# Kernel tuning notes

Measured on AMD Instinct MI355X. Metric: run time of the kernel, lower is better.

The kernel has to match this reference:

```python
import jax, jax.numpy as jnp
import numpy as np

N_WIRES = 4
N_LAYERS = 2
PATCHES = 196  # 14x14 grid of 2x2 patches


def _bexp(a, nd):
    # broadcast angle to rank nd by appending singleton axes
    a = jnp.asarray(a)
    return a.reshape(a.shape + (1,) * (nd - a.ndim))


def _apply_ry(state, wire, angle):
    # state: [B, P, 2,2,2,2]; angle broadcastable to [B, P] or scalar
    st = jnp.moveaxis(state, 2 + wire, -1)
    c = _bexp(jnp.cos(angle * 0.5), st.ndim - 1)
    s = _bexp(jnp.sin(angle * 0.5), st.ndim - 1)
    s0, s1 = st[..., 0], st[..., 1]
    out = jnp.stack([c * s0 - s * s1, s * s0 + c * s1], axis=-1)
    return jnp.moveaxis(out, -1, 2 + wire)


def _apply_cnot(state, control, target):
    st = jnp.moveaxis(state, (2 + control, 2 + target), (-2, -1))
    st = jnp.stack([st[..., 0, :], st[..., 1, ::-1]], axis=-2)
    return jnp.moveaxis(st, (-2, -1), (2 + control, 2 + target))


def _measure_z(state):
    # PauliZ expectation on each wire: sum probs * (+1/-1)
    p = state * state  # real state => |amp|^2
    outs = []
    for w in range(N_WIRES):
        axes = tuple(a for a in range(2, 2 + N_WIRES) if a != 2 + w)
        m = p.sum(axis=axes)  # [B, P, 2]
        outs.append(m[..., 0] - m[..., 1])
    return jnp.stack(outs, axis=-1)  # [B, P, 4]


def _quanv(x, theta):
    B = x.shape[0]
    # extract 2x2 patches: order (r,c),(r,c+1),(r+1,c),(r+1,c+1)
    img = x.reshape(B, 14, 2, 14, 2).transpose(0, 1, 3, 2, 4).reshape(B, PATCHES, 4)
    state = jnp.zeros((B, PATCHES, 16), x.dtype).at[:, :, 0].set(1.0)
    state = state.reshape(B, PATCHES, 2, 2, 2, 2)
    # encoder: RY(x_i) on wire i
    for w in range(N_WIRES):
        state = _apply_ry(state, w, img[:, :, w])
    # variational layers: trainable RY per wire + CNOT ring
    for l in range(N_LAYERS):
        for w in range(N_WIRES):
            state = _apply_ry(state, w, theta[l, w])
        for w in range(N_WIRES):
            state = _apply_cnot(state, w, (w + 1) % N_WIRES)
    return _measure_z(state).reshape(B, PATCHES * N_WIRES)  # [B, 784]


def setup_inputs() -> dict:
    key = jax.random.key(0)
    k = jax.random.split(key, 6)
    B = 4096
    return {
        "x": jax.random.uniform(k[0], (B, 784), jnp.float32),
        "theta": jax.random.normal(k[1], (N_LAYERS, N_WIRES), jnp.float32),
        "W1": jax.random.normal(k[2], (784, 128), jnp.float32) * 0.05,
        "b1": jnp.zeros((128,), jnp.float32),
        "W2": jax.random.normal(k[3], (128, 10), jnp.float32) * 0.05,
        "b2": jnp.zeros((10,), jnp.float32),
    }


def reference(x, theta, W1, b1, W2, b2):
    feats = _quanv(x, theta)                 # [B, 784]
    h = jax.nn.relu(feats @ W1 + b1)          # [B, 128]
    logits = h @ W2 + b2                      # [B, 10]
    return jax.nn.log_softmax(logits, axis=-1)
```

## Files before the change

kernel.cpp:

```cpp
#include <hip/hip_runtime.h>
#include <math.h>

#define PATCHES 196
#define KPAD 800
#define MROWS 16
#define CIRC (MROWS * PATCHES)
#define FRAG_ELEMS (25 * 64 * 8)

typedef short short8 __attribute__((ext_vector_type(8)));
typedef float f32x4 __attribute__((ext_vector_type(4)));

__device__ __forceinline__ unsigned short f2bf(float f) {
  union { float f; unsigned u; } x; x.f = f;
  unsigned r = x.u + 0x7fff + ((x.u >> 16) & 1);
  return (unsigned short)(r >> 16);
}

__global__ __launch_bounds__(256) void w1t_pack_kernel(
    const float* __restrict__ W1, unsigned short* __restrict__ w1p) {
  int idx = blockIdx.x * 256 + threadIdx.x;
  if (idx >= 128 * KPAD) return;
  int n = idx / KPAD;
  int k = idx - n * KPAD;
  float v = (k < 784) ? W1[k * 128 + n] : 0.f;
  int ki = k >> 5;
  int quad = (k & 31) >> 3;
  int j = k & 7;
  w1p[(n >> 4) * FRAG_ELEMS + (ki * 64 + quad * 16 + (n & 15)) * 8 + j] = f2bf(v);
}

__device__ __forceinline__ void apply_ry(float st[16], int bit, float c, float s) {
#pragma unroll
  for (int i = 0; i < 16; ++i) {
    if (!(i & bit)) {
      int j = i | bit;
      float a0 = st[i], a1 = st[j];
      st[i] = c * a0 - s * a1;
      st[j] = s * a0 + c * a1;
    }
  }
}

__device__ __forceinline__ void apply_cnot(float st[16], int cb, int tb) {
#pragma unroll
  for (int i = 0; i < 16; ++i) {
    if ((i & cb) && !(i & tb)) {
      int j = i | tb;
      float t = st[i]; st[i] = st[j]; st[j] = t;
    }
  }
}

__global__ __launch_bounds__(1024) void fused_kernel(
    const float* __restrict__ x, const float* __restrict__ theta,
    const unsigned short* __restrict__ w1p, const float* __restrict__ b1,
    const float* __restrict__ W2, const float* __restrict__ b2,
    float* __restrict__ out) {
  __shared__ unsigned short afr[FRAG_ELEMS];
  __shared__ float tc[8], ts[8];
  __shared__ float hs[MROWS * 132];
  __shared__ float ls[MROWS * 10];

  const int tid = threadIdx.x;
  const int row0 = blockIdx.x * MROWS;

  if (tid < 8) {
    float a = 0.5f * theta[tid];
    tc[tid] = __cosf(a);
    ts[tid] = __sinf(a);
  }
  if (tid < 64) {
    int m = tid & 15;
    int qs = tid >> 4;
    int quad = 2 + (qs >> 1);
    int j0 = (qs & 1) * 4;
    ushort4 z; z.x = z.y = z.z = z.w = 0;
    *reinterpret_cast<ushort4*>(afr + (24 * 64 + quad * 16 + m) * 8 + j0) = z;
  }
  __syncthreads();

  for (int c = tid; c < CIRC; c += 1024) {
    int bl = c / PATCHES;
    int p = c - bl * PATCHES;
    int pr = p / 14;
    int pc = p - pr * 14;

    const float* xb = x + (size_t)(row0 + bl) * 784 + pr * 56 + pc * 2;
    float v0 = xb[0], v1 = xb[1], v2 = xb[28], v3 = xb[29];

    float st[16];
#pragma unroll
    for (int i = 0; i < 16; ++i) st[i] = 0.f;
    st[0] = 1.f;

    apply_ry(st, 8, __cosf(0.5f * v0), __sinf(0.5f * v0));
    apply_ry(st, 4, __cosf(0.5f * v1), __sinf(0.5f * v1));
    apply_ry(st, 2, __cosf(0.5f * v2), __sinf(0.5f * v2));
    apply_ry(st, 1, __cosf(0.5f * v3), __sinf(0.5f * v3));

#pragma unroll
    for (int l = 0; l < 2; ++l) {
      apply_ry(st, 8, tc[l * 4 + 0], ts[l * 4 + 0]);
      apply_ry(st, 4, tc[l * 4 + 1], ts[l * 4 + 1]);
      apply_ry(st, 2, tc[l * 4 + 2], ts[l * 4 + 2]);
      apply_ry(st, 1, tc[l * 4 + 3], ts[l * 4 + 3]);
      apply_cnot(st, 8, 4);
      apply_cnot(st, 4, 2);
      apply_cnot(st, 2, 1);
      apply_cnot(st, 1, 8);
    }

    float m0 = 0.f, m1 = 0.f, m2 = 0.f, m3 = 0.f;
#pragma unroll
    for (int i = 0; i < 16; ++i) {
      float p2 = st[i] * st[i];
      m0 += (i & 8) ? -p2 : p2;
      m1 += (i & 4) ? -p2 : p2;
      m2 += (i & 2) ? -p2 : p2;
      m3 += (i & 1) ? -p2 : p2;
    }

    int K = p * 4;
    int ki = K >> 5;
    int quad = (K & 31) >> 3;
    int j0 = K & 7;
    ushort4 o;
    o.x = f2bf(m0); o.y = f2bf(m1); o.z = f2bf(m2); o.w = f2bf(m3);
    *reinterpret_cast<ushort4*>(afr + (ki * 64 + quad * 16 + bl) * 8 + j0) = o;
  }
  __syncthreads();

  const int lane = tid & 63;
  const int wave = tid >> 6;
  const int m = lane & 15;
  const int quad = lane >> 4;

  if (wave < 8) {
    const unsigned short* bp = w1p + (size_t)wave * FRAG_ELEMS + lane * 8;
    const unsigned short* apl = afr + lane * 8;

    f32x4 acc = {0.f, 0.f, 0.f, 0.f};

#pragma unroll
    for (int kc = 0; kc < 5; ++kc) {
      short8 a[5], b[5];
#pragma unroll
      for (int u = 0; u < 5; ++u) {
        const int ki = kc * 5 + u;
        a[u] = *reinterpret_cast<const short8*>(apl + ki * 512);
        b[u] = *reinterpret_cast<const short8*>(bp + ki * 512);
      }
#pragma unroll
      for (int u = 0; u < 5; ++u)
        acc = __builtin_amdgcn_mfma_f32_16x16x32_bf16(a[u], b[u], acc, 0, 0, 0);
    }

    const int col = wave * 16 + m;
    const float bc = b1[col];
#pragma unroll
    for (int r = 0; r < 4; ++r)
      hs[(quad * 4 + r) * 132 + col] = fmaxf(acc[r] + bc, 0.f);
  }
  __syncthreads();

  if (tid < MROWS * 10) {
    const int r = tid / 10;
    const int k = tid - r * 10;
    float a = b2[k];
    const float* hr = hs + r * 132;
#pragma unroll 8
    for (int jj = 0; jj < 128; ++jj) a = fmaf(hr[jj], W2[jj * 10 + k], a);
    ls[tid] = a;
  }
  __syncthreads();

  if (tid < MROWS) {
    const int r = tid;
    float mx = ls[r * 10];
#pragma unroll
    for (int k = 1; k < 10; ++k) mx = fmaxf(mx, ls[r * 10 + k]);
    float sum = 0.f;
#pragma unroll
    for (int k = 0; k < 10; ++k) sum += __expf(ls[r * 10 + k] - mx);
    const float lse = mx + __logf(sum);
    float* orow = out + (size_t)(row0 + r) * 10;
#pragma unroll
    for (int k = 0; k < 10; ++k) orow[k] = ls[r * 10 + k] - lse;
  }
}

extern "C" void kernel_launch(void* const* d_in, const int* in_sizes, int n_in,
                              void* d_out, int out_size, void* d_ws, size_t ws_size,
                              hipStream_t stream) {
  const float* x     = (const float*)d_in[0];
  const float* theta = (const float*)d_in[1];
  const float* W1    = (const float*)d_in[2];
  const float* b1    = (const float*)d_in[3];
  const float* W2    = (const float*)d_in[4];
  const float* b2    = (const float*)d_in[5];
  float* out = (float*)d_out;

  const int B = in_sizes[0] / 784;

  unsigned short* w1p = (unsigned short*)d_ws;

  w1t_pack_kernel<<<(128 * KPAD + 255) / 256, 256, 0, stream>>>(W1, w1p);
  fused_kernel<<<B / MROWS, 1024, 0, stream>>>(x, theta, w1p, b1, W2, b2, out);
}
```

Baseline: 89.49 us.

## Halve rows per block, prefetch inputs into registers, stage W2 in LDS

```diff
diff --git a/kernel.cpp b/kernel.cpp
--- a/kernel.cpp
+++ b/kernel.cpp
@@ -3,8 +3,9 @@
 
 #define PATCHES 196
 #define KPAD 800
-#define MROWS 16
+#define MROWS 8
 #define CIRC (MROWS * PATCHES)
+#define THREADS 512
 #define FRAG_ELEMS (25 * 64 * 8)
 
 typedef short short8 __attribute__((ext_vector_type(8)));
@@ -51,46 +52,61 @@
   }
 }
 
-__global__ __launch_bounds__(1024) void fused_kernel(
+__global__ __launch_bounds__(THREADS) void fused_kernel(
     const float* __restrict__ x, const float* __restrict__ theta,
     const unsigned short* __restrict__ w1p, const float* __restrict__ b1,
     const float* __restrict__ W2, const float* __restrict__ b2,
     float* __restrict__ out) {
   __shared__ unsigned short afr[FRAG_ELEMS];
   __shared__ float tc[8], ts[8];
+  __shared__ float ws2[1280];
   __shared__ float hs[MROWS * 132];
   __shared__ float ls[MROWS * 10];
 
   const int tid = threadIdx.x;
   const int row0 = blockIdx.x * MROWS;
 
+  {
+    ushort4 z; z.x = z.y = z.z = z.w = 0;
+    for (int s = tid; s < FRAG_ELEMS / 4; s += THREADS)
+      reinterpret_cast<ushort4*>(afr)[s] = z;
+  }
   if (tid < 8) {
     float a = 0.5f * theta[tid];
     tc[tid] = __cosf(a);
     ts[tid] = __sinf(a);
   }
-  if (tid < 64) {
-    int m = tid & 15;
-    int qs = tid >> 4;
-    int quad = 2 + (qs >> 1);
-    int j0 = (qs & 1) * 4;
-    ushort4 z; z.x = z.y = z.z = z.w = 0;
-    *reinterpret_cast<ushort4*>(afr + (24 * 64 + quad * 16 + m) * 8 + j0) = z;
-  }
-  __syncthreads();
-
-  for (int c = tid; c < CIRC; c += 1024) {
+  if (tid < 320)
+    reinterpret_cast<float4*>(ws2)[tid] = reinterpret_cast<const float4*>(W2)[tid];
+
+  const int nit = (tid + 3 * THREADS < CIRC) ? 4 : 3;
+  float2 xa[4], xb2[4];
+#pragma unroll
+  for (int i = 0; i < 4; ++i) {
+    if (i < nit) {
+      int c = tid + i * THREADS;
+      int bl = c / PATCHES;
+      int p = c - bl * PATCHES;
+      int pr = p / 14;
+      int pc = p - pr * 14;
+      const float* xb = x + (size_t)(row0 + bl) * 784 + pr * 56 + pc * 2;
+      xa[i]  = *reinterpret_cast<const float2*>(xb);
+      xb2[i] = *reinterpret_cast<const float2*>(xb + 28);
+    }
+  }
+  __syncthreads();
+
+#pragma unroll
+  for (int i = 0; i < 4; ++i) {
+    if (i >= nit) break;
+    int c = tid + i * THREADS;
     int bl = c / PATCHES;
     int p = c - bl * PATCHES;
-    int pr = p / 14;
-    int pc = p - pr * 14;
-
-    const float* xb = x + (size_t)(row0 + bl) * 784 + pr * 56 + pc * 2;
-    float v0 = xb[0], v1 = xb[1], v2 = xb[28], v3 = xb[29];
+    float v0 = xa[i].x, v1 = xa[i].y, v2 = xb2[i].x, v3 = xb2[i].y;
 
     float st[16];
 #pragma unroll
-    for (int i = 0; i < 16; ++i) st[i] = 0.f;
+    for (int q = 0; q < 16; ++q) st[q] = 0.f;
     st[0] = 1.f;
 
     apply_ry(st, 8, __cosf(0.5f * v0), __sinf(0.5f * v0));
@@ -112,12 +128,12 @@
 
     float m0 = 0.f, m1 = 0.f, m2 = 0.f, m3 = 0.f;
 #pragma unroll
-    for (int i = 0; i < 16; ++i) {
-      float p2 = st[i] * st[i];
-      m0 += (i & 8) ? -p2 : p2;
-      m1 += (i & 4) ? -p2 : p2;
-      m2 += (i & 2) ? -p2 : p2;
-      m3 += (i & 1) ? -p2 : p2;
+    for (int q = 0; q < 16; ++q) {
+      float p2 = st[q] * st[q];
+      m0 += (q & 8) ? -p2 : p2;
+      m1 += (q & 4) ? -p2 : p2;
+      m2 += (q & 2) ? -p2 : p2;
+      m3 += (q & 1) ? -p2 : p2;
     }
 
     int K = p * 4;
@@ -135,7 +151,7 @@
   const int m = lane & 15;
   const int quad = lane >> 4;
 
-  if (wave < 8) {
+  {
     const unsigned short* bp = w1p + (size_t)wave * FRAG_ELEMS + lane * 8;
     const unsigned short* apl = afr + lane * 8;
 
@@ -155,11 +171,13 @@
         acc = __builtin_amdgcn_mfma_f32_16x16x32_bf16(a[u], b[u], acc, 0, 0, 0);
     }
 
-    const int col = wave * 16 + m;
-    const float bc = b1[col];
-#pragma unroll
-    for (int r = 0; r < 4; ++r)
-      hs[(quad * 4 + r) * 132 + col] = fmaxf(acc[r] + bc, 0.f);
+    if (quad < 2) {
+      const int col = wave * 16 + m;
+      const float bc = b1[col];
+#pragma unroll
+      for (int r = 0; r < 4; ++r)
+        hs[(quad * 4 + r) * 132 + col] = fmaxf(acc[r] + bc, 0.f);
+    }
   }
   __syncthreads();
 
@@ -169,7 +187,7 @@
     float a = b2[k];
     const float* hr = hs + r * 132;
 #pragma unroll 8
-    for (int jj = 0; jj < 128; ++jj) a = fmaf(hr[jj], W2[jj * 10 + k], a);
+    for (int jj = 0; jj < 128; ++jj) a = fmaf(hr[jj], ws2[jj * 10 + k], a);
     ls[tid] = a;
   }
   __syncthreads();
@@ -205,5 +223,5 @@
   unsigned short* w1p = (unsigned short*)d_ws;
 
   w1t_pack_kernel<<<(128 * KPAD + 255) / 256, 256, 0, stream>>>(W1, w1p);
-  fused_kernel<<<B / MROWS, 1024, 0, stream>>>(x, theta, w1p, b1, W2, b2, out);
-}
+  fused_kernel<<<B / MROWS, THREADS, 0, stream>>>(x, theta, w1p, b1, W2, b2, out);
+}
```

After: 86.00 us. 1.04x faster.
